# Optimization experiments

Measured on AMD Instinct MI355X. Metric: run time of the kernel, lower is better.

Reference implementation:

```python
import jax, jax.numpy as jnp
import numpy as np

N_NODES = 100000
N_EDGES = 300000
IN_CH = 256
HID = 256


def setup_inputs() -> dict:
    key = jax.random.key(0)
    k1, k2, k3, k4 = jax.random.split(key, 4)
    z = jax.random.normal(k1, (N_NODES, IN_CH), dtype=jnp.float32)
    edge_index = jax.random.randint(k2, (2, N_EDGES), 0, N_NODES, dtype=jnp.int64)
    # Linear params (torch default init ~ U(-1/sqrt(fan_in), 1/sqrt(fan_in)))
    b1s = 1.0 / np.sqrt(2 * IN_CH)
    b2s = 1.0 / np.sqrt(HID)
    W1 = jax.random.uniform(k3, (HID, 2 * IN_CH), minval=-b1s, maxval=b1s, dtype=jnp.float32)
    b1 = jnp.zeros((HID,), dtype=jnp.float32)
    W2 = jax.random.uniform(k4, (1, HID), minval=-b2s, maxval=b2s, dtype=jnp.float32)
    b2 = jnp.zeros((1,), dtype=jnp.float32)
    return {"z": z, "W1": W1, "b1": b1, "W2": W2, "b2": b2, "edge_index": edge_index}


def reference(z, W1, b1, W2, b2, edge_index):
    # Gather src/dst node embeddings: [E, D] each
    src = z[edge_index[0]]
    dst = z[edge_index[1]]
    # Avoid materializing concat by splitting W1 into src/dst halves:
    # lin1(cat([src,dst])) == src @ W1[:, :D].T + dst @ W1[:, D:].T + b1
    W1s, W1d = W1[:, :IN_CH], W1[:, IN_CH:]
    h = jnp.einsum('ed,hd->eh', src, W1s) + jnp.einsum('ed,hd->eh', dst, W1d) + b1
    h = jax.nn.relu(h)
    out = jnp.einsum('eh,oh->eo', h, W2) + b2  # [E, 1]
    return out[:, 0]
```

## Files before the change

### kernel.cpp

```cpp
#include <hip/hip_runtime.h>


#define NN 100000
#define NE 300000
#define KD 256
#define NO 512
#define BN 128

typedef __attribute__((ext_vector_type(8))) short short8;
typedef __attribute__((ext_vector_type(8))) unsigned short ushort8;
typedef __attribute__((ext_vector_type(4))) float f32x4;
typedef __attribute__((ext_vector_type(4))) unsigned int uint4v;

__device__ __forceinline__ unsigned short f2bf(float f) {
  union { float f; unsigned int u; } v; v.f = f;
  unsigned int u = v.u;
  u += 0x7fffu + ((u >> 16) & 1u);
  return (unsigned short)(u >> 16);
}
__device__ __forceinline__ float bf2f(unsigned short h) {
  union { unsigned int u; float f; } v; v.u = ((unsigned int)h) << 16;
  return v.f;
}
__device__ __forceinline__ unsigned int pkbf(float a, float b) {
  unsigned int ua = __float_as_uint(a) + 0x8000u;
  unsigned int ub = __float_as_uint(b) + 0x8000u;
  return __builtin_amdgcn_perm(ub, ua, 0x07060302u);
}
__device__ __forceinline__ int hperm(int s) {
  int j = s & 127;
  return (s & ~127) + ((j & 7) << 4) + (j >> 3);
}

__global__ void prep_w(const float* __restrict__ W1, unsigned short* __restrict__ Wt) {
  int idx = blockIdx.x * 256 + threadIdx.x;
  int j = idx >> 8, k = idx & 255;
  float v = (j < 256) ? W1[j * 512 + k] : W1[(j - 256) * 512 + 256 + k];
  Wt[idx] = f2bf(v);
}

__global__ __launch_bounds__(256, 2) void gemm_zw(const float* __restrict__ z,
                                                  const unsigned short* __restrict__ Wt,
                                                  unsigned short* __restrict__ C) {
  __shared__ unsigned short Bs[BN * KD];

  const int b = blockIdx.x;
  const int xcd = b & 7;
  const int s = b >> 3;
  const int nt = s & 3;
  const int mg = xcd * 32 + (s >> 2);
  const int n0 = nt * BN;

  const int t = threadIdx.x;
  const int w = t >> 6, lane = t & 63;
  const int l15 = lane & 15, l4 = lane >> 4;

  for (int i = 0; i < 16; ++i) {
    const int id = t + 256 * i;
    const int row = id >> 5, c = id & 31;
    ushort8 v = *(const ushort8*)(Wt + (size_t)(n0 + row) * KD + c * 8);
    *(ushort8*)&Bs[row * KD + ((c ^ (row & 7)) << 3)] = v;
  }
  __syncthreads();

  const int strm = mg * 4 + w;

  for (int g = 0; g < 4; ++g) {
    const int b0 = strm + 2048 * g;
    if (b0 >= 6250) break;
    int b1 = b0 + 1024;
    if (b1 >= 6250) b1 = b0;

    f32x4 acc0[8], acc1[8];
#pragma unroll
    for (int n = 0; n < 8; ++n) { acc0[n] = (f32x4)0.f; acc1[n] = (f32x4)0.f; }

    const float* z0 = z + ((size_t)b0 * 16 + l15) * KD + l4 * 8;
    const float* z1 = z + ((size_t)b1 * 16 + l15) * KD + l4 * 8;

#pragma unroll
    for (int ks = 0; ks < 8; ++ks) {
      const float4 a0 = *(const float4*)(z0 + ks * 32);
      const float4 a0b = *(const float4*)(z0 + ks * 32 + 4);
      const float4 a1 = *(const float4*)(z1 + ks * 32);
      const float4 a1b = *(const float4*)(z1 + ks * 32 + 4);
      union { uint4v u; short8 s; } c0v, c1v;
      c0v.u[0] = pkbf(a0.x, a0.y);  c0v.u[1] = pkbf(a0.z, a0.w);
      c0v.u[2] = pkbf(a0b.x, a0b.y); c0v.u[3] = pkbf(a0b.z, a0b.w);
      c1v.u[0] = pkbf(a1.x, a1.y);  c1v.u[1] = pkbf(a1.z, a1.w);
      c1v.u[2] = pkbf(a1b.x, a1b.y); c1v.u[3] = pkbf(a1b.z, a1b.w);
#pragma unroll
      for (int n = 0; n < 8; ++n) {
        union { ushort8 u; short8 s; } bv;
        bv.u = *(const ushort8*)&Bs[(n * 16 + l15) * KD +
                                    (((ks * 4 + l4) ^ (l15 & 7)) << 3)];
        acc0[n] = __builtin_amdgcn_mfma_f32_16x16x32_bf16(c0v.s, bv.s, acc0[n], 0, 0, 0);
        acc1[n] = __builtin_amdgcn_mfma_f32_16x16x32_bf16(c1v.s, bv.s, acc1[n], 0, 0, 0);
      }
    }

#pragma unroll
    for (int r = 0; r < 4; ++r) {
      uint4v q;
      q[0] = pkbf(acc0[0][r], acc0[1][r]); q[1] = pkbf(acc0[2][r], acc0[3][r]);
      q[2] = pkbf(acc0[4][r], acc0[5][r]); q[3] = pkbf(acc0[6][r], acc0[7][r]);
      *(uint4v*)(C + ((size_t)b0 * 16 + l4 * 4 + r) * NO + n0 + l15 * 8) = q;
      q[0] = pkbf(acc1[0][r], acc1[1][r]); q[1] = pkbf(acc1[2][r], acc1[3][r]);
      q[2] = pkbf(acc1[4][r], acc1[5][r]); q[3] = pkbf(acc1[6][r], acc1[7][r]);
      *(uint4v*)(C + ((size_t)b1 * 16 + l4 * 4 + r) * NO + n0 + l15 * 8) = q;
    }
  }
}

__global__ __launch_bounds__(256) void edge_mlp(const unsigned short* __restrict__ C,
                                                const int* __restrict__ ei,
                                                const float* __restrict__ b1,
                                                const float* __restrict__ W2,
                                                const float* __restrict__ b2,
                                                float* __restrict__ out) {
  const int t = threadIdx.x;
  const int lane = t & 63;
  const int g = lane >> 4;
  const int c0 = (lane & 15) * 16;
  float b1v[16], w2v[16];
#pragma unroll
  for (int i = 0; i < 16; ++i) {
    const int h = hperm(c0 + i);
    b1v[i] = b1[h]; w2v[i] = W2[h];
  }
  const float bias2 = b2[0];
  const int waveId = blockIdx.x * 4 + (t >> 6);
  const int nw = gridDim.x * 4;
  for (int e0 = waveId * 4; e0 < NE; e0 += nw * 4) {
    const int e = e0 + g;
    const int sn = ei[e];
    const int dn = ei[NE + e];
    const ushort8* ap = (const ushort8*)(C + (size_t)sn * NO + c0);
    const ushort8* bp = (const ushort8*)(C + (size_t)dn * NO + 256 + c0);
    ushort8 a0 = ap[0], a1 = ap[1];
    ushort8 v0 = bp[0], v1 = bp[1];
    float partial = 0.f;
#pragma unroll
    for (int j = 0; j < 8; ++j) {
      float h = bf2f(a0[j]) + bf2f(v0[j]) + b1v[j];
      h = fmaxf(h, 0.f);
      partial = fmaf(h, w2v[j], partial);
    }
#pragma unroll
    for (int j = 0; j < 8; ++j) {
      float h = bf2f(a1[j]) + bf2f(v1[j]) + b1v[8 + j];
      h = fmaxf(h, 0.f);
      partial = fmaf(h, w2v[8 + j], partial);
    }
    partial += __shfl_xor(partial, 8);
    partial += __shfl_xor(partial, 4);
    partial += __shfl_xor(partial, 2);
    partial += __shfl_xor(partial, 1);
    if ((lane & 15) == 0) out[e] = partial + bias2;
  }
}

extern "C" void kernel_launch(void* const* d_in, const int* in_sizes, int n_in,
                              void* d_out, int out_size, void* d_ws, size_t ws_size,
                              hipStream_t stream) {
  const float* z  = (const float*)d_in[0];
  const float* W1 = (const float*)d_in[1];
  const float* b1 = (const float*)d_in[2];
  const float* W2 = (const float*)d_in[3];
  const float* b2 = (const float*)d_in[4];
  const int*   ei = (const int*)d_in[5];
  float* out = (float*)d_out;

  unsigned short* C  = (unsigned short*)d_ws;
  unsigned short* Wt = C + (size_t)NN * NO;

  prep_w<<<512, 256, 0, stream>>>(W1, Wt);
  gemm_zw<<<1024, 256, 0, stream>>>(z, Wt, C);
  edge_mlp<<<2048, 256, 0, stream>>>(C, ei, b1, W2, b2, out);
}
```

Measured before the change: 124.4 us.

## Restructure node GEMM: one 32-node tile per wave, prefetched z loads, natural output layout

The node-embedding GEMM no longer loops over several node groups per wave. It now launches enough blocks for each wave to handle exactly one 32-node tile, and the MFMA operands are swapped so the output lands in natural column order, removing the hperm index permutation in the edge kernel. z loads are software-pipelined two k-steps ahead, with sched barriers, to hide global latency behind MFMAs. The trade-off is more blocks that each reload the 64KB weight tile into LDS, and narrower 8-byte output stores.

```diff
diff --git a/kernel.cpp b/kernel.cpp
--- a/kernel.cpp
+++ b/kernel.cpp
@@ -5,7 +5,6 @@
 #define NE 300000
 #define KD 256
 #define NO 512
-#define BN 128
 
 typedef __attribute__((ext_vector_type(8))) short short8;
 typedef __attribute__((ext_vector_type(8))) unsigned short ushort8;
@@ -27,10 +26,6 @@
   unsigned int ub = __float_as_uint(b) + 0x8000u;
   return __builtin_amdgcn_perm(ub, ua, 0x07060302u);
 }
-__device__ __forceinline__ int hperm(int s) {
-  int j = s & 127;
-  return (s & ~127) + ((j & 7) << 4) + (j >> 3);
-}
 
 __global__ void prep_w(const float* __restrict__ W1, unsigned short* __restrict__ Wt) {
   int idx = blockIdx.x * 256 + threadIdx.x;
@@ -42,19 +37,21 @@
 __global__ __launch_bounds__(256, 2) void gemm_zw(const float* __restrict__ z,
                                                   const unsigned short* __restrict__ Wt,
                                                   unsigned short* __restrict__ C) {
-  __shared__ unsigned short Bs[BN * KD];
+  __shared__ unsigned short Bs[128 * KD];
 
   const int b = blockIdx.x;
   const int xcd = b & 7;
-  const int s = b >> 3;
-  const int nt = s & 3;
-  const int mg = xcd * 32 + (s >> 2);
-  const int n0 = nt * BN;
+  const int rr = b >> 3;
+  const int q = rr & 3;
+  const int g = (rr >> 2) * 8 + xcd;
+  if (g >= 782) return;
+  const int n0 = q * 128;
 
   const int t = threadIdx.x;
   const int w = t >> 6, lane = t & 63;
   const int l15 = lane & 15, l4 = lane >> 4;
 
+#pragma unroll
   for (int i = 0; i < 16; ++i) {
     const int id = t + 256 * i;
     const int row = id >> 5, c = id & 31;
@@ -63,52 +60,66 @@
   }
   __syncthreads();
 
-  const int strm = mg * 4 + w;
+  const int slot = g * 4 + w;
+  if (slot >= 3125) return;
+  const int node0 = slot * 32;
 
-  for (int g = 0; g < 4; ++g) {
-    const int b0 = strm + 2048 * g;
-    if (b0 >= 6250) break;
-    int b1 = b0 + 1024;
-    if (b1 >= 6250) b1 = b0;
+  const float* zr = z + (size_t)(node0 + l15) * KD + l4 * 8;
 
-    f32x4 acc0[8], acc1[8];
+#define LOADZ(kc, Ra, Rb, Rc, Rd)                                  \
+  Ra = *(const float4*)(zr + (kc) * 32);                           \
+  Rb = *(const float4*)(zr + (kc) * 32 + 4);                       \
+  Rc = *(const float4*)(zr + 16 * KD + (kc) * 32);                 \
+  Rd = *(const float4*)(zr + 16 * KD + (kc) * 32 + 4);
+
+  float4 Z0a, Z0b, Z0c, Z0d, Z1a, Z1b, Z1c, Z1d;
+  LOADZ(0, Z0a, Z0b, Z0c, Z0d)
+  LOADZ(1, Z1a, Z1b, Z1c, Z1d)
+  __builtin_amdgcn_sched_barrier(0);
+
+  f32x4 acc0[8], acc1[8];
 #pragma unroll
-    for (int n = 0; n < 8; ++n) { acc0[n] = (f32x4)0.f; acc1[n] = (f32x4)0.f; }
+  for (int f = 0; f < 8; ++f) { acc0[f] = (f32x4)0.f; acc1[f] = (f32x4)0.f; }
 
-    const float* z0 = z + ((size_t)b0 * 16 + l15) * KD + l4 * 8;
-    const float* z1 = z + ((size_t)b1 * 16 + l15) * KD + l4 * 8;
+#define KSTEP(kc, Ra, Rb, Rc, Rd, PF)                                   \
+  {                                                                     \
+    union { uint4v u; short8 s; } zb0, zb1;                             \
+    zb0.u[0] = pkbf(Ra.x, Ra.y); zb0.u[1] = pkbf(Ra.z, Ra.w);           \
+    zb0.u[2] = pkbf(Rb.x, Rb.y); zb0.u[3] = pkbf(Rb.z, Rb.w);           \
+    zb1.u[0] = pkbf(Rc.x, Rc.y); zb1.u[1] = pkbf(Rc.z, Rc.w);           \
+    zb1.u[2] = pkbf(Rd.x, Rd.y); zb1.u[3] = pkbf(Rd.z, Rd.w);           \
+    if (PF) { LOADZ((kc) + 2, Ra, Rb, Rc, Rd)                           \
+              __builtin_amdgcn_sched_barrier(0); }                      \
+    _Pragma("unroll")                                                   \
+    for (int f = 0; f < 8; ++f) {                                       \
+      union { ushort8 u; short8 s; } wv;                                \
+      wv.u = *(const ushort8*)&Bs[(f * 16 + l15) * KD +                 \
+                                  ((((kc) * 4 + l4) ^ (l15 & 7)) << 3)];\
+      acc0[f] = __builtin_amdgcn_mfma_f32_16x16x32_bf16(wv.s, zb0.s, acc0[f], 0, 0, 0); \
+      acc1[f] = __builtin_amdgcn_mfma_f32_16x16x32_bf16(wv.s, zb1.s, acc1[f], 0, 0, 0); \
+    }                                                                   \
+  }
+
+  KSTEP(0, Z0a, Z0b, Z0c, Z0d, 1)
+  KSTEP(1, Z1a, Z1b, Z1c, Z1d, 1)
+  KSTEP(2, Z0a, Z0b, Z0c, Z0d, 1)
+  KSTEP(3, Z1a, Z1b, Z1c, Z1d, 1)
+  KSTEP(4, Z0a, Z0b, Z0c, Z0d, 1)
+  KSTEP(5, Z1a, Z1b, Z1c, Z1d, 1)
+  KSTEP(6, Z0a, Z0b, Z0c, Z0d, 0)
+  KSTEP(7, Z1a, Z1b, Z1c, Z1d, 0)
+#undef KSTEP
+#undef LOADZ
 
 #pragma unroll
-    for (int ks = 0; ks < 8; ++ks) {
-      const float4 a0 = *(const float4*)(z0 + ks * 32);
-      const float4 a0b = *(const float4*)(z0 + ks * 32 + 4);
-      const float4 a1 = *(const float4*)(z1 + ks * 32);
-      const float4 a1b = *(const float4*)(z1 + ks * 32 + 4);
-      union { uint4v u; short8 s; } c0v, c1v;
-      c0v.u[0] = pkbf(a0.x, a0.y);  c0v.u[1] = pkbf(a0.z, a0.w);
-      c0v.u[2] = pkbf(a0b.x, a0b.y); c0v.u[3] = pkbf(a0b.z, a0b.w);
-      c1v.u[0] = pkbf(a1.x, a1.y);  c1v.u[1] = pkbf(a1.z, a1.w);
-      c1v.u[2] = pkbf(a1b.x, a1b.y); c1v.u[3] = pkbf(a1b.z, a1b.w);
-#pragma unroll
-      for (int n = 0; n < 8; ++n) {
-        union { ushort8 u; short8 s; } bv;
-        bv.u = *(const ushort8*)&Bs[(n * 16 + l15) * KD +
-                                    (((ks * 4 + l4) ^ (l15 & 7)) << 3)];
-        acc0[n] = __builtin_amdgcn_mfma_f32_16x16x32_bf16(c0v.s, bv.s, acc0[n], 0, 0, 0);
-        acc1[n] = __builtin_amdgcn_mfma_f32_16x16x32_bf16(c1v.s, bv.s, acc1[n], 0, 0, 0);
-      }
-    }
-
-#pragma unroll
-    for (int r = 0; r < 4; ++r) {
-      uint4v q;
-      q[0] = pkbf(acc0[0][r], acc0[1][r]); q[1] = pkbf(acc0[2][r], acc0[3][r]);
-      q[2] = pkbf(acc0[4][r], acc0[5][r]); q[3] = pkbf(acc0[6][r], acc0[7][r]);
-      *(uint4v*)(C + ((size_t)b0 * 16 + l4 * 4 + r) * NO + n0 + l15 * 8) = q;
-      q[0] = pkbf(acc1[0][r], acc1[1][r]); q[1] = pkbf(acc1[2][r], acc1[3][r]);
-      q[2] = pkbf(acc1[4][r], acc1[5][r]); q[3] = pkbf(acc1[6][r], acc1[7][r]);
-      *(uint4v*)(C + ((size_t)b1 * 16 + l4 * 4 + r) * NO + n0 + l15 * 8) = q;
-    }
+  for (int f = 0; f < 8; ++f) {
+    uint2 p;
+    p.x = pkbf(acc0[f][0], acc0[f][1]);
+    p.y = pkbf(acc0[f][2], acc0[f][3]);
+    *(uint2*)(C + (size_t)(node0 + l15) * NO + n0 + f * 16 + l4 * 4) = p;
+    p.x = pkbf(acc1[f][0], acc1[f][1]);
+    p.y = pkbf(acc1[f][2], acc1[f][3]);
+    *(uint2*)(C + (size_t)(node0 + 16 + l15) * NO + n0 + f * 16 + l4 * 4) = p;
   }
 }
 
@@ -124,10 +135,7 @@
   const int c0 = (lane & 15) * 16;
   float b1v[16], w2v[16];
 #pragma unroll
-  for (int i = 0; i < 16; ++i) {
-    const int h = hperm(c0 + i);
-    b1v[i] = b1[h]; w2v[i] = W2[h];
-  }
+  for (int i = 0; i < 16; ++i) { b1v[i] = b1[c0 + i]; w2v[i] = W2[c0 + i]; }
   const float bias2 = b2[0];
   const int waveId = blockIdx.x * 4 + (t >> 6);
   const int nw = gridDim.x * 4;
@@ -175,6 +183,6 @@
   unsigned short* Wt = C + (size_t)NN * NO;
 
   prep_w<<<512, 256, 0, stream>>>(W1, Wt);
-  gemm_zw<<<1024, 256, 0, stream>>>(z, Wt, C);
+  gemm_zw<<<3136, 256, 0, stream>>>(z, Wt, C);
   edge_mlp<<<2048, 256, 0, stream>>>(C, ei, b1, W2, b2, out);
 }
```

After: 126.4 us. About the same (+1.6%).
